# Performance work log

Measured on AMD Instinct MI355X. Metric: run time of the kernel, lower is better.

Reference implementation:

```python
import jax, jax.numpy as jnp
import numpy as np

NEIGHBOR_K = 3


def setup_inputs() -> dict:
    key = jax.random.key(0)
    k1, k2 = jax.random.split(key)
    x1 = jax.random.normal(k1, (64, 640, 441), dtype=jnp.float32)   # [B, C, l] queries
    x2 = jax.random.normal(k2, (32, 640, 2205), dtype=jnp.float32)  # [N, C, m] support classes
    return {"x1": x1, "x2": x2}


def reference(x1, x2):
    # x1: [B, C, l] query local descriptors; x2: [N, C, m] support-class descriptors
    q = jnp.swapaxes(x1, 1, 2)                                   # [B, l, C]
    q = q / jnp.linalg.norm(q, axis=-1, keepdims=True)           # L2-normalize each descriptor
    s = x2 / jnp.linalg.norm(x2, axis=1, keepdims=True)          # normalize each support column over C

    def per_class(sj):                                            # sj: [C, m]
        scores = jnp.einsum('blc,cm->blm', q, sj)                # [B, l, m] cosine sims
        topk_vals = jax.lax.top_k(scores, NEIGHBOR_K)[0]         # [B, l, k] top-k over support descriptors
        return jnp.sum(topk_vals, axis=(1, 2))                   # [B] image-to-class similarity

    # map over support classes to avoid materializing [B, N, l, m]
    sims = jax.lax.map(per_class, s)                              # [N, B]
    return sims.T                                                 # [B, N]
```

## Files before the change

kernel.cpp:

```cpp
#include <hip/hip_runtime.h>
#include <hip/hip_bf16.h>
#include <float.h>

#define BQ    64
#define CDIM  640
#define LQ    441
#define NCLS  32
#define MS    2205
#define ITILES 7
#define JCHUNK 256
#define NJC    9
#define NKC    10
#define NEG_INF (-3.0e38f)

#define ABYTES 81920
#define ADW    20480
#define BMC    327680
#define BN     (NJC * BMC)

typedef __attribute__((ext_vector_type(8))) short short8;
typedef __attribute__((ext_vector_type(4))) float f32x4;

__device__ __forceinline__ void ins3(float s, float& a, float& b, float& c) {
  float na = fmaxf(a, s);
  float nb = __builtin_amdgcn_fmed3f(a, b, s);
  c = fmaxf(c, fminf(b, s));
  a = na; b = nb;
}

__global__ __launch_bounds__(1024) void prep_q(const float* __restrict__ x1,
                                               unsigned short* __restrict__ Abf) {
  const int it = blockIdx.x;
  const int b  = blockIdx.y;
  const int t  = threadIdx.x;
  const int il = t & 63, cg = t >> 6;
  __shared__ float red[16][64];
  __shared__ float rnq[64];
  __shared__ unsigned short tile[64][66];

  const int i = it * 64 + il;
  float ss = 0.f;
  if (i < LQ) {
    for (int c = cg; c < CDIM; c += 16) {
      float v = x1[((size_t)b * CDIM + c) * LQ + i];
      ss += v * v;
    }
  }
  red[cg][il] = ss;
  __syncthreads();
  if (t < 64) {
    float s = 0.f;
    #pragma unroll
    for (int g = 0; g < 16; ++g) s += red[g][t];
    rnq[t] = (it * 64 + t < LQ) ? rsqrtf(s) : 0.f;
  }
  __syncthreads();

  unsigned int* blob = (unsigned int*)Abf + (size_t)(b * ITILES + it) * ADW;
  for (int kc = 0; kc < NKC; ++kc) {
    for (int idx = t; idx < 4096; idx += 1024) {
      int cc = idx >> 6, ii = idx & 63;
      int gi = it * 64 + ii;
      float v = 0.f;
      if (gi < LQ) v = x1[((size_t)b * CDIM + kc * 64 + cc) * LQ + gi] * rnq[ii];
      __hip_bfloat16 h = __float2bfloat16(v);
      tile[cc][ii] = *(unsigned short*)&h;
    }
    __syncthreads();
    for (int idx = t; idx < 2048; idx += 1024) {
      int row = idx >> 5, kp = idx & 31;
      unsigned int lo = tile[kp * 2][row], hi = tile[kp * 2 + 1][row];
      blob[row * 320 + kc * 32 + kp] = lo | (hi << 16);
    }
    __syncthreads();
  }
}

__global__ __launch_bounds__(1024) void prep_s(const float* __restrict__ x2,
                                               char* __restrict__ Bbf) {
  const int mc = blockIdx.x;
  const int n  = blockIdx.y;
  const int t  = threadIdx.x;
  const int jj = t & 255, cg = t >> 8;
  __shared__ float red[4][256];
  __shared__ float rns[256];
  __shared__ unsigned short tile[64][266];

  const int j = mc * 256 + jj;
  float ss = 0.f;
  if (j < MS) {
    for (int c = cg; c < CDIM; c += 4) {
      float v = x2[((size_t)n * CDIM + c) * MS + j];
      ss += v * v;
    }
  }
  red[cg][jj] = ss;
  __syncthreads();
  if (t < 256) {
    float s = red[0][t] + red[1][t] + red[2][t] + red[3][t];
    rns[t] = (mc * 256 + t < MS) ? rsqrtf(s) : 0.f;
  }
  __syncthreads();

  char* blob = Bbf + ((size_t)n * NJC + mc) * BMC;
  for (int kc = 0; kc < NKC; ++kc) {
    for (int idx = t; idx < 16384; idx += 1024) {
      int cc = idx >> 8, jc = idx & 255;
      int gj = mc * 256 + jc;
      float v = 0.f;
      if (gj < MS) v = x2[((size_t)n * CDIM + kc * 64 + cc) * MS + gj] * rns[jc];
      __hip_bfloat16 h = __float2bfloat16(v);
      tile[cc][jc] = *(unsigned short*)&h;
    }
    __syncthreads();
    for (int g = t; g < 2048; g += 1024) {
      int ks = g >> 10, jf = (g >> 6) & 15, ln = g & 63;
      int qq = ln >> 4, cl = ln & 15;
      int col = jf * 16 + cl, k0 = ks * 32 + qq * 8;
      unsigned int u0 = (unsigned int)tile[k0 + 0][col] | ((unsigned int)tile[k0 + 1][col] << 16);
      unsigned int u1 = (unsigned int)tile[k0 + 2][col] | ((unsigned int)tile[k0 + 3][col] << 16);
      unsigned int u2 = (unsigned int)tile[k0 + 4][col] | ((unsigned int)tile[k0 + 5][col] << 16);
      unsigned int u3 = (unsigned int)tile[k0 + 6][col] | ((unsigned int)tile[k0 + 7][col] << 16);
      int4 w; w.x = u0; w.y = u1; w.z = u2; w.w = u3;
      *(int4*)(blob + (size_t)kc * 32768 + (size_t)g * 16) = w;
    }
    __syncthreads();
  }
}

__global__ __launch_bounds__(256, 2) void gemm_topk(const int4* __restrict__ Abf,
                                                    const char* __restrict__ Bbf,
                                                    float* __restrict__ out) {
  const int bid = blockIdx.x;
  const int xcd = bid & 7;
  const int s   = bid >> 3;
  const int n   = xcd * 4 + s / 448;
  const int bx  = s % 448;
  const int b   = bx / 7;
  const int t    = threadIdx.x;
  const int lane = t & 63, wave = t >> 6;
  const int l15  = lane & 15, q = lane >> 4;

  __shared__ __align__(16) char smem[ABYTES];

  {
    const int4* gA = Abf + (size_t)bx * 5120;
    int4* sA = (int4*)smem;
    #pragma unroll
    for (int rep = 0; rep < 20; ++rep) {
      int g0 = t + rep * 256;
      int i = g0 / 80;
      int g = g0 - i * 80;
      sA[i * 80 + (g ^ (i & 7))] = gA[g0];
    }
  }
  __syncthreads();

  float t3[16][3];
  #pragma unroll
  for (int r = 0; r < 16; ++r) { t3[r][0] = NEG_INF; t3[r][1] = NEG_INF; t3[r][2] = NEG_INF; }

  const int swz  = l15 & 7;
  const int oct0 = (q ^ swz) * 16;
  const int oct1 = ((4 + q) ^ swz) * 16;
  const char* Ab = smem + l15 * 1280;
  const int jb = wave * 64 + l15;

  const char* BnB = Bbf + (size_t)n * BN + wave * 4096 + lane * 16;

  short8 bcur[2][4], bnxt[2][4];
  int off = 0;
  #pragma unroll
  for (int ks = 0; ks < 2; ++ks)
    #pragma unroll
    for (int c = 0; c < 4; ++c)
      bcur[ks][c] = *(const short8*)(BnB + ks * 16384 + c * 1024);

  for (int mc = 0; mc < NJC; ++mc) {
    f32x4 acc[4][4];
    #pragma unroll
    for (int r = 0; r < 4; ++r)
      #pragma unroll
      for (int c = 0; c < 4; ++c) acc[r][c] = (f32x4){0.f, 0.f, 0.f, 0.f};

    #pragma unroll 2
    for (int kc = 0; kc < NKC; ++kc) {
      int offn = off + 32768;
      if (offn == BN) offn = 0;
      #pragma unroll
      for (int ks = 0; ks < 2; ++ks)
        #pragma unroll
        for (int c = 0; c < 4; ++c)
          bnxt[ks][c] = *(const short8*)(BnB + offn + ks * 16384 + c * 1024);

      __builtin_amdgcn_s_setprio(1);
      #pragma unroll
      for (int ks = 0; ks < 2; ++ks) {
        const int oct = ks ? oct1 : oct0;
        short8 af[4];
        #pragma unroll
        for (int r = 0; r < 4; ++r)
          af[r] = *(const short8*)(Ab + r * 20480 + kc * 128 + oct);
        #pragma unroll
        for (int r = 0; r < 4; ++r)
          #pragma unroll
          for (int c = 0; c < 4; ++c)
            acc[r][c] = __builtin_amdgcn_mfma_f32_16x16x32_bf16(af[r], bcur[ks][c], acc[r][c], 0, 0, 0);
      }
      __builtin_amdgcn_s_setprio(0);

      #pragma unroll
      for (int ks = 0; ks < 2; ++ks)
        #pragma unroll
        for (int c = 0; c < 4; ++c) bcur[ks][c] = bnxt[ks][c];
      off = offn;
    }

    #pragma unroll
    for (int c = 0; c < 4; ++c) {
      const bool jv = (mc * JCHUNK + c * 16 + jb) < MS;
      #pragma unroll
      for (int r = 0; r < 4; ++r)
        #pragma unroll
        for (int reg = 0; reg < 4; ++reg) {
          float sv = jv ? acc[r][c][reg] : NEG_INF;
          ins3(sv, t3[r * 4 + reg][0], t3[r * 4 + reg][1], t3[r * 4 + reg][2]);
        }
    }
  }

  __syncthreads();
  float* mrg = (float*)smem;
  float* aux = (float*)(smem + 49920);
  #pragma unroll
  for (int r = 0; r < 4; ++r)
    #pragma unroll
    for (int reg = 0; reg < 4; ++reg) {
      int row = r * 16 + q * 4 + reg;
      int col = wave * 16 + l15;
      float* p = &mrg[(row * 65 + col) * 3];
      p[0] = t3[r * 4 + reg][0]; p[1] = t3[r * 4 + reg][1]; p[2] = t3[r * 4 + reg][2];
    }
  __syncthreads();
  {
    int row = t >> 2, seg = t & 3;
    float a = NEG_INF, bb = NEG_INF, cc = NEG_INF;
    for (int c0 = seg * 16; c0 < seg * 16 + 16; ++c0) {
      const float* p = &mrg[(row * 65 + c0) * 3];
      ins3(p[0], a, bb, cc); ins3(p[1], a, bb, cc); ins3(p[2], a, bb, cc);
    }
    aux[(row * 4 + seg) * 3 + 0] = a;
    aux[(row * 4 + seg) * 3 + 1] = bb;
    aux[(row * 4 + seg) * 3 + 2] = cc;
  }
  __syncthreads();
  if (t < 64) {
    float a = NEG_INF, bb = NEG_INF, cc = NEG_INF;
    for (int v = 0; v < 12; ++v) ins3(aux[t * 12 + v], a, bb, cc);
    float sum = a + bb + cc;
    for (int offr = 32; offr > 0; offr >>= 1) sum += __shfl_down(sum, offr);
    if (t == 0) atomicAdd(&out[b * NCLS + n], sum);
  }
}

extern "C" void kernel_launch(void* const* d_in, const int* in_sizes, int n_in,
                              void* d_out, int out_size, void* d_ws, size_t ws_size,
                              hipStream_t stream) {
  const float* x1 = (const float*)d_in[0];
  const float* x2 = (const float*)d_in[1];
  float* out = (float*)d_out;

  unsigned short* Abf = (unsigned short*)d_ws;
  char* Bbf = (char*)d_ws + (size_t)BQ * ITILES * ABYTES;

  hipMemsetAsync(d_out, 0, BQ * NCLS * sizeof(float), stream);
  prep_q<<<dim3(ITILES, BQ), 1024, 0, stream>>>(x1, Abf);
  prep_s<<<dim3(NJC, NCLS), 1024, 0, stream>>>(x2, Bbf);
  gemm_topk<<<BQ * ITILES * NCLS, 256, 0, stream>>>((const int4*)Abf, Bbf, out);
}
```

Measured before the change: 2.680 ms.

## Widen GEMM-topk blocks to 12 waves splitting support chunks three ways

Each block now runs 768 threads (12 waves). The nine 256-column support chunks are split across three wave groups, so each wave loops over 3 chunks instead of 9 while sharing the same LDS-resident query tile. The cross-wave top-3 merge is serialized over the three groups with extra barriers. This cuts the redundant per-block A staging relative to compute and raises the waves per CU, at the cost of register pressure under the 768x3 launch bound and a longer merge epilogue.

Measured after the change: 3.369 ms. 1.26x slower.

```diff
diff --git a/kernel.cpp b/kernel.cpp
--- a/kernel.cpp
+++ b/kernel.cpp
@@ -8,8 +8,8 @@
 #define NCLS  32
 #define MS    2205
 #define ITILES 7
-#define JCHUNK 256
 #define NJC    9
+#define NMC   3
 #define NKC    10
 #define NEG_INF (-3.0e38f)
 
@@ -128,7 +128,7 @@
   }
 }
 
-__global__ __launch_bounds__(256, 2) void gemm_topk(const int4* __restrict__ Abf,
+__global__ __launch_bounds__(768, 3) void gemm_topk(const int4* __restrict__ Abf,
                                                     const char* __restrict__ Bbf,
                                                     float* __restrict__ out) {
   const int bid = blockIdx.x;
@@ -146,9 +146,7 @@
   {
     const int4* gA = Abf + (size_t)bx * 5120;
     int4* sA = (int4*)smem;
-    #pragma unroll
-    for (int rep = 0; rep < 20; ++rep) {
-      int g0 = t + rep * 256;
+    for (int g0 = t; g0 < 5120; g0 += 768) {
       int i = g0 / 80;
       int g = g0 - i * 80;
       sA[i * 80 + (g ^ (i & 7))] = gA[g0];
@@ -166,17 +164,17 @@
   const char* Ab = smem + l15 * 1280;
   const int jb = wave * 64 + l15;
 
-  const char* BnB = Bbf + (size_t)n * BN + wave * 4096 + lane * 16;
+  const char* Bp = Bbf + (size_t)n * BN + (size_t)(wave >> 2) * BMC
+                   + (size_t)(wave & 3) * 4096 + (size_t)lane * 16;
 
   short8 bcur[2][4], bnxt[2][4];
-  int off = 0;
   #pragma unroll
   for (int ks = 0; ks < 2; ++ks)
     #pragma unroll
     for (int c = 0; c < 4; ++c)
-      bcur[ks][c] = *(const short8*)(BnB + ks * 16384 + c * 1024);
-
-  for (int mc = 0; mc < NJC; ++mc) {
+      bcur[ks][c] = *(const short8*)(Bp + ks * 16384 + c * 1024);
+
+  for (int mc = 0; mc < NMC; ++mc) {
     f32x4 acc[4][4];
     #pragma unroll
     for (int r = 0; r < 4; ++r)
@@ -185,13 +183,12 @@
 
     #pragma unroll 2
     for (int kc = 0; kc < NKC; ++kc) {
-      int offn = off + 32768;
-      if (offn == BN) offn = 0;
+      int poff = (kc < 9) ? (kc + 1) * 32768 : ((mc < NMC - 1) ? 3 * BMC : kc * 32768);
       #pragma unroll
       for (int ks = 0; ks < 2; ++ks)
         #pragma unroll
         for (int c = 0; c < 4; ++c)
-          bnxt[ks][c] = *(const short8*)(BnB + offn + ks * 16384 + c * 1024);
+          bnxt[ks][c] = *(const short8*)(Bp + poff + ks * 16384 + c * 1024);
 
       __builtin_amdgcn_s_setprio(1);
       #pragma unroll
@@ -213,12 +210,12 @@
       for (int ks = 0; ks < 2; ++ks)
         #pragma unroll
         for (int c = 0; c < 4; ++c) bcur[ks][c] = bnxt[ks][c];
-      off = offn;
-    }
+    }
+    Bp += 3 * BMC;
 
     #pragma unroll
     for (int c = 0; c < 4; ++c) {
-      const bool jv = (mc * JCHUNK + c * 16 + jb) < MS;
+      const bool jv = (mc * 768 + c * 16 + jb) < MS;
       #pragma unroll
       for (int r = 0; r < 4; ++r)
         #pragma unroll
@@ -232,31 +229,38 @@
   __syncthreads();
   float* mrg = (float*)smem;
   float* aux = (float*)(smem + 49920);
-  #pragma unroll
-  for (int r = 0; r < 4; ++r)
-    #pragma unroll
-    for (int reg = 0; reg < 4; ++reg) {
-      int row = r * 16 + q * 4 + reg;
-      int col = wave * 16 + l15;
-      float* p = &mrg[(row * 65 + col) * 3];
-      p[0] = t3[r * 4 + reg][0]; p[1] = t3[r * 4 + reg][1]; p[2] = t3[r * 4 + reg][2];
-    }
-  __syncthreads();
-  {
-    int row = t >> 2, seg = t & 3;
-    float a = NEG_INF, bb = NEG_INF, cc = NEG_INF;
-    for (int c0 = seg * 16; c0 < seg * 16 + 16; ++c0) {
-      const float* p = &mrg[(row * 65 + c0) * 3];
-      ins3(p[0], a, bb, cc); ins3(p[1], a, bb, cc); ins3(p[2], a, bb, cc);
-    }
-    aux[(row * 4 + seg) * 3 + 0] = a;
-    aux[(row * 4 + seg) * 3 + 1] = bb;
-    aux[(row * 4 + seg) * 3 + 2] = cc;
-  }
-  __syncthreads();
+  const int g12 = wave >> 2;
+  const int w4  = wave & 3;
+  for (int g = 0; g < 3; ++g) {
+    if (g12 == g) {
+      #pragma unroll
+      for (int r = 0; r < 4; ++r)
+        #pragma unroll
+        for (int reg = 0; reg < 4; ++reg) {
+          int row = r * 16 + q * 4 + reg;
+          int col = w4 * 16 + l15;
+          float* p = &mrg[(row * 65 + col) * 3];
+          p[0] = t3[r * 4 + reg][0]; p[1] = t3[r * 4 + reg][1]; p[2] = t3[r * 4 + reg][2];
+        }
+    }
+    __syncthreads();
+    if (g12 == g) {
+      int tg = t & 255;
+      int row = tg >> 2, seg = tg & 3;
+      float a = NEG_INF, bb = NEG_INF, cc = NEG_INF;
+      for (int c0 = seg * 16; c0 < seg * 16 + 16; ++c0) {
+        const float* p = &mrg[(row * 65 + c0) * 3];
+        ins3(p[0], a, bb, cc); ins3(p[1], a, bb, cc); ins3(p[2], a, bb, cc);
+      }
+      aux[(row * 12 + g * 4 + seg) * 3 + 0] = a;
+      aux[(row * 12 + g * 4 + seg) * 3 + 1] = bb;
+      aux[(row * 12 + g * 4 + seg) * 3 + 2] = cc;
+    }
+    __syncthreads();
+  }
   if (t < 64) {
     float a = NEG_INF, bb = NEG_INF, cc = NEG_INF;
-    for (int v = 0; v < 12; ++v) ins3(aux[t * 12 + v], a, bb, cc);
+    for (int v = 0; v < 36; ++v) ins3(aux[t * 36 + v], a, bb, cc);
     float sum = a + bb + cc;
     for (int offr = 32; offr > 0; offr >>= 1) sum += __shfl_down(sum, offr);
     if (t == 0) atomicAdd(&out[b * NCLS + n], sum);
@@ -276,5 +280,5 @@
   hipMemsetAsync(d_out, 0, BQ * NCLS * sizeof(float), stream);
   prep_q<<<dim3(ITILES, BQ), 1024, 0, stream>>>(x1, Abf);
   prep_s<<<dim3(NJC, NCLS), 1024, 0, stream>>>(x2, Bbf);
-  gemm_topk<<<BQ * ITILES * NCLS, 256, 0, stream>>>((const int4*)Abf, Bbf, out);
-}
+  gemm_topk<<<BQ * ITILES * NCLS, 768, 0, stream>>>((const int4*)Abf, Bbf, out);
+}
```

## Split prep kernels into norm and layout passes; manually double-buffer B loads

Applied to the files above, without the earlier changes.

Splits each preprocessing kernel into a norm kernel that writes inverse norms to workspace and a layout kernel parallelised over K-chunks. This gives far more blocks than the old prep_s grid of 288 blocks, which looped serially over 10 chunks. The GEMM inner loop is hand-unrolled by two with explicit ping-pong B register buffers, removing the register copy from the next buffer to the current one. The split path costs extra kernel launches and a second read of x1 and x2, and it falls back to the old kernels if the workspace is too small.

New measurement: 7.533 ms. 2.81x slower.

```diff
diff --git a/kernel.cpp b/kernel.cpp
--- a/kernel.cpp
+++ b/kernel.cpp
@@ -28,6 +28,116 @@
   a = na; b = nb;
 }
 
+
+__global__ __launch_bounds__(1024) void norm_q(const float* __restrict__ x1,
+                                               float* __restrict__ rnq_g) {
+  const int it = blockIdx.x, b = blockIdx.y;
+  const int t = threadIdx.x;
+  const int il = t & 63, cg = t >> 6;
+  __shared__ float red[16][64];
+  const int i = it * 64 + il;
+  float ss = 0.f;
+  if (i < LQ) {
+    for (int c = cg; c < CDIM; c += 16) {
+      float v = x1[((size_t)b * CDIM + c) * LQ + i];
+      ss += v * v;
+    }
+  }
+  red[cg][il] = ss;
+  __syncthreads();
+  if (t < 64) {
+    float s = 0.f;
+    #pragma unroll
+    for (int g = 0; g < 16; ++g) s += red[g][t];
+    rnq_g[(b * ITILES + it) * 64 + t] = (it * 64 + t < LQ) ? rsqrtf(s) : 0.f;
+  }
+}
+
+__global__ __launch_bounds__(256) void layout_q(const float* __restrict__ x1,
+                                                const float* __restrict__ rnq_g,
+                                                unsigned short* __restrict__ Abf) {
+  const int kc = blockIdx.x;
+  const int bx = blockIdx.y;
+  const int it = bx % ITILES, b = bx / ITILES;
+  const int t = threadIdx.x;
+  __shared__ unsigned short tile[64][66];
+  __shared__ float rnq[64];
+  if (t < 64) rnq[t] = rnq_g[bx * 64 + t];
+  __syncthreads();
+  for (int idx = t; idx < 4096; idx += 256) {
+    int cc = idx >> 6, ii = idx & 63;
+    int gi = it * 64 + ii;
+    float v = 0.f;
+    if (gi < LQ) v = x1[((size_t)b * CDIM + kc * 64 + cc) * LQ + gi] * rnq[ii];
+    __hip_bfloat16 h = __float2bfloat16(v);
+    tile[cc][ii] = *(unsigned short*)&h;
+  }
+  __syncthreads();
+  unsigned int* blob = (unsigned int*)Abf + (size_t)bx * ADW;
+  for (int idx = t; idx < 2048; idx += 256) {
+    int row = idx >> 5, kp = idx & 31;
+    unsigned int lo = tile[kp * 2][row], hi = tile[kp * 2 + 1][row];
+    blob[row * 320 + kc * 32 + kp] = lo | (hi << 16);
+  }
+}
+
+__global__ __launch_bounds__(1024) void norm_s(const float* __restrict__ x2,
+                                               float* __restrict__ rns_g) {
+  const int mc = blockIdx.x, n = blockIdx.y;
+  const int t = threadIdx.x;
+  const int jj = t & 255, cg = t >> 8;
+  __shared__ float red[4][256];
+  const int j = mc * 256 + jj;
+  float ss = 0.f;
+  if (j < MS) {
+    for (int c = cg; c < CDIM; c += 4) {
+      float v = x2[((size_t)n * CDIM + c) * MS + j];
+      ss += v * v;
+    }
+  }
+  red[cg][jj] = ss;
+  __syncthreads();
+  if (t < 256) {
+    float s = red[0][t] + red[1][t] + red[2][t] + red[3][t];
+    rns_g[n * 2304 + mc * 256 + t] = (mc * 256 + t < MS) ? rsqrtf(s) : 0.f;
+  }
+}
+
+__global__ __launch_bounds__(512) void layout_s(const float* __restrict__ x2,
+                                                const float* __restrict__ rns_g,
+                                                char* __restrict__ Bbf) {
+  const int kc = blockIdx.x;
+  const int mc = blockIdx.y;
+  const int n  = blockIdx.z;
+  const int t = threadIdx.x;
+  __shared__ unsigned short tile[64][266];
+  __shared__ float rns[256];
+  if (t < 256) rns[t] = rns_g[n * 2304 + mc * 256 + t];
+  __syncthreads();
+  for (int idx = t; idx < 16384; idx += 512) {
+    int cc = idx >> 8, jc = idx & 255;
+    int gj = mc * 256 + jc;
+    float v = 0.f;
+    if (gj < MS) v = x2[((size_t)n * CDIM + kc * 64 + cc) * MS + gj] * rns[jc];
+    __hip_bfloat16 h = __float2bfloat16(v);
+    tile[cc][jc] = *(unsigned short*)&h;
+  }
+  __syncthreads();
+  char* blob = Bbf + ((size_t)n * NJC + mc) * BMC + (size_t)kc * 32768;
+  for (int g = t; g < 2048; g += 512) {
+    int ks = g >> 10, jf = (g >> 6) & 15, ln = g & 63;
+    int qq = ln >> 4, cl = ln & 15;
+    int col = jf * 16 + cl, k0 = ks * 32 + qq * 8;
+    unsigned int u0 = (unsigned int)tile[k0 + 0][col] | ((unsigned int)tile[k0 + 1][col] << 16);
+    unsigned int u1 = (unsigned int)tile[k0 + 2][col] | ((unsigned int)tile[k0 + 3][col] << 16);
+    unsigned int u2 = (unsigned int)tile[k0 + 4][col] | ((unsigned int)tile[k0 + 5][col] << 16);
+    unsigned int u3 = (unsigned int)tile[k0 + 6][col] | ((unsigned int)tile[k0 + 7][col] << 16);
+    int4 w; w.x = u0; w.y = u1; w.z = u2; w.w = u3;
+    *(int4*)(blob + (size_t)g * 16) = w;
+  }
+}
+
+
 __global__ __launch_bounds__(1024) void prep_q(const float* __restrict__ x1,
                                                unsigned short* __restrict__ Abf) {
   const int it = blockIdx.x;
@@ -37,7 +147,6 @@
   __shared__ float red[16][64];
   __shared__ float rnq[64];
   __shared__ unsigned short tile[64][66];
-
   const int i = it * 64 + il;
   float ss = 0.f;
   if (i < LQ) {
@@ -55,7 +164,6 @@
     rnq[t] = (it * 64 + t < LQ) ? rsqrtf(s) : 0.f;
   }
   __syncthreads();
-
   unsigned int* blob = (unsigned int*)Abf + (size_t)(b * ITILES + it) * ADW;
   for (int kc = 0; kc < NKC; ++kc) {
     for (int idx = t; idx < 4096; idx += 1024) {
@@ -85,7 +193,6 @@
   __shared__ float red[4][256];
   __shared__ float rns[256];
   __shared__ unsigned short tile[64][266];
-
   const int j = mc * 256 + jj;
   float ss = 0.f;
   if (j < MS) {
@@ -98,10 +205,9 @@
   __syncthreads();
   if (t < 256) {
     float s = red[0][t] + red[1][t] + red[2][t] + red[3][t];
-    rns[t] = (mc * 256 + t < MS) ? rsqrtf(s) : 0.f;
-  }
-  __syncthreads();
-
+    rns[t] = (mc * 256 + t < MS) ? rsqrtf(ss = s) : 0.f;
+  }
+  __syncthreads();
   char* blob = Bbf + ((size_t)n * NJC + mc) * BMC;
   for (int kc = 0; kc < NKC; ++kc) {
     for (int idx = t; idx < 16384; idx += 1024) {
@@ -168,13 +274,13 @@
 
   const char* BnB = Bbf + (size_t)n * BN + wave * 4096 + lane * 16;
 
-  short8 bcur[2][4], bnxt[2][4];
+  short8 b0[2][4], b1[2][4];
   int off = 0;
   #pragma unroll
   for (int ks = 0; ks < 2; ++ks)
     #pragma unroll
     for (int c = 0; c < 4; ++c)
-      bcur[ks][c] = *(const short8*)(BnB + ks * 16384 + c * 1024);
+      b0[ks][c] = *(const short8*)(BnB + ks * 16384 + c * 1024);
 
   for (int mc = 0; mc < NJC; ++mc) {
     f32x4 acc[4][4];
@@ -183,15 +289,13 @@
       #pragma unroll
       for (int c = 0; c < 4; ++c) acc[r][c] = (f32x4){0.f, 0.f, 0.f, 0.f};
 
-    #pragma unroll 2
-    for (int kc = 0; kc < NKC; ++kc) {
-      int offn = off + 32768;
-      if (offn == BN) offn = 0;
+    for (int kc2 = 0; kc2 < NKC; kc2 += 2) {
+      int off1 = off + 32768; if (off1 == BN) off1 = 0;
       #pragma unroll
       for (int ks = 0; ks < 2; ++ks)
         #pragma unroll
         for (int c = 0; c < 4; ++c)
-          bnxt[ks][c] = *(const short8*)(BnB + offn + ks * 16384 + c * 1024);
+          b1[ks][c] = *(const short8*)(BnB + off1 + ks * 16384 + c * 1024);
 
       __builtin_amdgcn_s_setprio(1);
       #pragma unroll
@@ -200,20 +304,39 @@
         short8 af[4];
         #pragma unroll
         for (int r = 0; r < 4; ++r)
-          af[r] = *(const short8*)(Ab + r * 20480 + kc * 128 + oct);
+          af[r] = *(const short8*)(Ab + r * 20480 + kc2 * 128 + oct);
         #pragma unroll
         for (int r = 0; r < 4; ++r)
           #pragma unroll
           for (int c = 0; c < 4; ++c)
-            acc[r][c] = __builtin_amdgcn_mfma_f32_16x16x32_bf16(af[r], bcur[ks][c], acc[r][c], 0, 0, 0);
+            acc[r][c] = __builtin_amdgcn_mfma_f32_16x16x32_bf16(af[r], b0[ks][c], acc[r][c], 0, 0, 0);
       }
       __builtin_amdgcn_s_setprio(0);
 
+      int off2 = off1 + 32768; if (off2 == BN) off2 = 0;
       #pragma unroll
       for (int ks = 0; ks < 2; ++ks)
         #pragma unroll
-        for (int c = 0; c < 4; ++c) bcur[ks][c] = bnxt[ks][c];
-      off = offn;
+        for (int c = 0; c < 4; ++c)
+          b0[ks][c] = *(const short8*)(BnB + off2 + ks * 16384 + c * 1024);
+
+      __builtin_amdgcn_s_setprio(1);
+      #pragma unroll
+      for (int ks = 0; ks < 2; ++ks) {
+        const int oct = ks ? oct1 : oct0;
+        short8 af[4];
+        #pragma unroll
+        for (int r = 0; r < 4; ++r)
+          af[r] = *(const short8*)(Ab + r * 20480 + (kc2 + 1) * 128 + oct);
+        #pragma unroll
+        for (int r = 0; r < 4; ++r)
+          #pragma unroll
+          for (int c = 0; c < 4; ++c)
+            acc[r][c] = __builtin_amdgcn_mfma_f32_16x16x32_bf16(af[r], b1[ks][c], acc[r][c], 0, 0, 0);
+      }
+      __builtin_amdgcn_s_setprio(0);
+
+      off = off2;
     }
 
     #pragma unroll
@@ -270,11 +393,24 @@
   const float* x2 = (const float*)d_in[1];
   float* out = (float*)d_out;
 
+  const size_t abytes_tot = (size_t)BQ * ITILES * ABYTES;
+  const size_t bbytes_tot = (size_t)NCLS * BN;
   unsigned short* Abf = (unsigned short*)d_ws;
-  char* Bbf = (char*)d_ws + (size_t)BQ * ITILES * ABYTES;
+  char* Bbf = (char*)d_ws + abytes_tot;
+  float* rnq_g = (float*)((char*)d_ws + abytes_tot + bbytes_tot);
+  float* rns_g = rnq_g + BQ * ITILES * 64;
+  const size_t need_split = abytes_tot + bbytes_tot
+                          + (size_t)(BQ * ITILES * 64 + NCLS * 2304) * sizeof(float);
 
   hipMemsetAsync(d_out, 0, BQ * NCLS * sizeof(float), stream);
-  prep_q<<<dim3(ITILES, BQ), 1024, 0, stream>>>(x1, Abf);
-  prep_s<<<dim3(NJC, NCLS), 1024, 0, stream>>>(x2, Bbf);
+  if (ws_size >= need_split) {
+    norm_q<<<dim3(ITILES, BQ), 1024, 0, stream>>>(x1, rnq_g);
+    norm_s<<<dim3(NJC, NCLS), 1024, 0, stream>>>(x2, rns_g);
+    layout_q<<<dim3(NKC, BQ * ITILES), 256, 0, stream>>>(x1, rnq_g, Abf);
+    layout_s<<<dim3(NKC, NJC, NCLS), 512, 0, stream>>>(x2, rns_g, Bbf);
+  } else {
+    prep_q<<<dim3(ITILES, BQ), 1024, 0, stream>>>(x1, Abf);
+    prep_s<<<dim3(NJC, NCLS), 1024, 0, stream>>>(x2, Bbf);
+  }
   gemm_topk<<<BQ * ITILES * NCLS, 256, 0, stream>>>((const int4*)Abf, Bbf, out);
 }
```
